# Kernel tuning notes

Hardware: AMD Instinct MI355X
Metric: run time of the kernel (lower is better)

Reference implementation:

```python
import jax, jax.numpy as jnp
import numpy as np

B, S, D, H, L, V = 4, 512, 1024, 16, 4, 32000
DH = D // H
LATENT_START, N_LATENT, LATENT_ID = 64, 6, 5


def _ln(x, g, b):
    m = x.mean(-1, keepdims=True)
    v = ((x - m) ** 2).mean(-1, keepdims=True)
    return (x - m) * jax.lax.rsqrt(v + 1e-5) * g + b


def _model(x_emb, pos_ids, pos_emb, Wqkv, Wo, W1, W2, ln1_g, ln1_b, ln2_g, ln2_b, lnf_g, lnf_b, lm_head):
    # x_emb: [B,T,D]; returns (last_hidden [B,T,D] after final LN, logits [B,T,V])
    b, T, _ = x_emb.shape
    x = x_emb + pos_emb[pos_ids]
    causal = jnp.tril(jnp.ones((T, T), bool))
    for l in range(L):
        h = _ln(x, ln1_g[l], ln1_b[l])
        q, k, v = jnp.split(h @ Wqkv[l], 3, axis=-1)
        q = q.reshape(b, T, H, DH).transpose(0, 2, 1, 3)
        k = k.reshape(b, T, H, DH).transpose(0, 2, 1, 3)
        v = v.reshape(b, T, H, DH).transpose(0, 2, 1, 3)
        scores = jnp.einsum('bhqd,bhkd->bhqk', q, k) / np.float32(np.sqrt(DH))
        scores = jnp.where(causal, scores, jnp.float32(-1e9))
        attn = jax.nn.softmax(scores, axis=-1)
        o = jnp.einsum('bhqk,bhkd->bhqd', attn, v).transpose(0, 2, 1, 3).reshape(b, T, D)
        x = x + o @ Wo[l]
        h2 = _ln(x, ln2_g[l], ln2_b[l])
        x = x + jax.nn.gelu(h2 @ W1[l]) @ W2[l]
    hid = _ln(x, lnf_g, lnf_b)  # GPT2 hidden_states[-1] is post ln_f
    return hid, hid @ lm_head


def setup_inputs() -> dict:
    key = jax.random.key(0)
    ks = jax.random.split(key, 10)
    input_ids = jax.random.randint(ks[0], (B, S), 0, V, dtype=jnp.int32)
    input_ids = input_ids.at[:, LATENT_START:LATENT_START + N_LATENT].set(LATENT_ID)
    attention_mask = jnp.ones((B, S), jnp.int32)
    labels = jax.random.randint(ks[1], (B, S), 0, V, dtype=jnp.int32)
    position_ids = jnp.broadcast_to(jnp.arange(S, dtype=jnp.int32), (B, S))
    s = 0.02
    return {
        'input_ids': input_ids, 'attention_mask': attention_mask,
        'labels': labels, 'position_ids': position_ids,
        'emb': jax.random.normal(ks[2], (V, D), jnp.float32) * s,
        'pos_emb': jax.random.normal(ks[3], (S, D), jnp.float32) * s,
        'Wqkv': jax.random.normal(ks[4], (L, D, 3 * D), jnp.float32) * s,
        'Wo': jax.random.normal(ks[5], (L, D, D), jnp.float32) * s,
        'W1': jax.random.normal(ks[6], (L, D, 4 * D), jnp.float32) * s,
        'W2': jax.random.normal(ks[7], (L, 4 * D, D), jnp.float32) * s,
        'ln1_g': jnp.ones((L, D), jnp.float32), 'ln1_b': jnp.zeros((L, D), jnp.float32),
        'ln2_g': jnp.ones((L, D), jnp.float32), 'ln2_b': jnp.zeros((L, D), jnp.float32),
        'lnf_g': jnp.ones((D,), jnp.float32), 'lnf_b': jnp.zeros((D,), jnp.float32),
        'lm_head': jax.random.normal(ks[8], (D, V), jnp.float32) * s,
    }


def reference(input_ids, attention_mask, labels, position_ids, emb, pos_emb, Wqkv, Wo, W1, W2, ln1_g, ln1_b, ln2_g, ln2_b, lnf_g, lnf_b, lm_head):
    params = (pos_emb, Wqkv, Wo, W1, W2, ln1_g, ln1_b, ln2_g, ln2_b, lnf_g, lnf_b, lm_head)
    inputs_embeds = emb[input_ids]  # [B,S,D]
    start, end = 0, LATENT_START
    logits_list = []
    for p in range(N_LATENT):  # iterative latent passes
        hid, lg = _model(inputs_embeds[:, :end], position_ids[:, :end], *params)
        logits_list.append(lg[:, start:end])
        pos = LATENT_START + p
        # vectorized scatter: splice previous-position hidden state into latent slot
        inputs_embeds = inputs_embeds.at[:, pos, :].set(hid[:, pos - 1, :])
        start, end = end, (S if p + 1 >= N_LATENT else end + 1)
    hid, lg = _model(inputs_embeds[:, :end], position_ids[:, :end], *params)
    logits_list.append(lg[:, start:end])
    logits = jnp.concatenate(logits_list, axis=1)  # [B,S,V]
    shift_logits = logits[:, :-1]
    shift_labels = labels[:, 1:]
    logp = jax.nn.log_softmax(shift_logits, axis=-1)
    loss = -jnp.take_along_axis(logp, shift_labels[..., None], axis=-1).mean()
    return loss, inputs_embeds, logits
```

## Files before the change

kernel.cpp:

```cpp
#include <hip/hip_runtime.h>

static constexpr int BB  = 4;
static constexpr int SS  = 512;
static constexpr int DD  = 1024;
static constexpr int HH  = 16;
static constexpr int LL  = 4;
static constexpr int VV  = 32000;
static constexpr int DHH = 64;
static constexpr int FFF = 4096;

typedef short bf16x8  __attribute__((ext_vector_type(8)));
typedef short bf16x4v __attribute__((ext_vector_type(4)));
typedef float f32x4   __attribute__((ext_vector_type(4)));

__device__ __forceinline__ float b2f(ushort u){
  union { float f; unsigned int u32; } x; x.u32 = ((unsigned int)u) << 16; return x.f;
}
__device__ __forceinline__ ushort f2b(float f){
  union { float f; unsigned int u32; } x; x.f = f;
  unsigned int u = x.u32;
  return (ushort)((u + 0x7FFFu + ((u >> 16) & 1u)) >> 16);
}

__global__ __launch_bounds__(256) void convT_k(const float* __restrict__ in, ushort* __restrict__ out,
                                               int K, int N, long inStride, long outStride)
{
  in  += (long)blockIdx.z * inStride;
  out += (long)blockIdx.z * outStride;
  __shared__ float tile[64][65];
  int n0 = blockIdx.x * 64, k0 = blockIdx.y * 64;
  int tid = threadIdx.x;
  int cc = tid & 63, rr = tid >> 6;
#pragma unroll
  for (int i = 0; i < 16; i++){
    int r = rr + i * 4;
    tile[r][cc] = in[(long)(k0 + r) * N + n0 + cc];
  }
  __syncthreads();
#pragma unroll
  for (int i = 0; i < 16; i++){
    int r = rr + i * 4;
    out[(long)(n0 + r) * K + k0 + cc] = f2b(tile[cc][r]);
  }
}

__global__ __launch_bounds__(256) void embed_k(const int* __restrict__ ids, const float* __restrict__ emb,
                                               const float* __restrict__ pe, float* __restrict__ x,
                                               float* __restrict__ oemb)
{
  int t = blockIdx.x, b = blockIdx.y, tid = threadIdx.x;
  int id = ids[b * SS + t];
  float4 ev = *((const float4*)(emb + (long)id * DD) + tid);
  float4 pv = *((const float4*)(pe  + (long)t  * DD) + tid);
  *((float4*)(x + (long)(t * BB + b) * DD) + tid) =
      make_float4(ev.x + pv.x, ev.y + pv.y, ev.z + pv.z, ev.w + pv.w);
  float* op = oemb + ((long)b * SS + t) * DD + tid * 4;
  op[0] = ev.x; op[1] = ev.y; op[2] = ev.z; op[3] = ev.w;
}

__global__ __launch_bounds__(256) void ln_k(const float* __restrict__ xin, const float* __restrict__ g,
                                            const float* __restrict__ bt, ushort* __restrict__ out, long row0)
{
  long row = row0 + blockIdx.x;
  int tid = threadIdx.x;
  const float* rp = xin + row * DD;
  float4 v = *(const float4*)(rp + tid * 4);
  float s1 = v.x + v.y + v.z + v.w;
  float s2 = v.x * v.x + v.y * v.y + v.z * v.z + v.w * v.w;
#pragma unroll
  for (int o = 32; o; o >>= 1){ s1 += __shfl_down(s1, o); s2 += __shfl_down(s2, o); }
  __shared__ float red[2][4];
  int wv = tid >> 6, lane = tid & 63;
  if (lane == 0){ red[0][wv] = s1; red[1][wv] = s2; }
  __syncthreads();
  s1 = red[0][0] + red[0][1] + red[0][2] + red[0][3];
  s2 = red[1][0] + red[1][1] + red[1][2] + red[1][3];
  float mean = s1 * (1.0f / DD);
  float var  = s2 * (1.0f / DD) - mean * mean;
  float rstd = rsqrtf(var + 1e-5f);
  float4 gv = *(const float4*)(g + tid * 4);
  float4 bv = *(const float4*)(bt + tid * 4);
  ushort4 o4;
  o4.x = f2b((v.x - mean) * rstd * gv.x + bv.x);
  o4.y = f2b((v.y - mean) * rstd * gv.y + bv.y);
  o4.z = f2b((v.z - mean) * rstd * gv.z + bv.z);
  o4.w = f2b((v.w - mean) * rstd * gv.w + bv.w);
  *(ushort4*)(out + row * DD + tid * 4) = o4;
}

template<int EPI>
__device__ __forceinline__ void epi_store(float v, int grow, int ocol, void* Cv, int ldc,
                                          const float* Add, int t0, int l,
                                          ushort* kc, ushort* vc, ushort* qb)
{
  if constexpr (EPI == 1){
    float* Cf = (float*)Cv; long idx = (long)grow * ldc + ocol;
    Cf[idx] = v + Add[idx];
  } else if constexpr (EPI == 2){
    ushort* Cb = (ushort*)Cv; long idx = (long)grow * ldc + ocol;
    float tt = 0.7978845608028654f * (v + 0.044715f * v * v * v);
    Cb[idx] = f2b(0.5f * v * (1.0f + tanhf(tt)));
  } else if constexpr (EPI == 3){
    int t = t0 + (grow >> 2), b = grow & 3;
    ((float*)Cv)[((long)b * SS + t) * VV + ocol] = v;
  } else if constexpr (EPI == 4){
    if (ocol < DD){
      qb[((long)(t0 * BB + grow)) * DD + ocol] = f2b(v);
    } else {
      int t = t0 + (grow >> 2), b = grow & 3;
      int h = (ocol >> 6) & 15, d = ocol & 63;
      long dst = (((long)l * BB + b) * HH + h) * ((long)SS * DHH) + (long)t * DHH + d;
      if (ocol >= 2 * DD) vc[dst] = f2b(v); else kc[dst] = f2b(v);
    }
  }
}

template<int EPI>
__global__ __launch_bounds__(256) void gemm_k(const ushort* __restrict__ A, int lda,
                                              const ushort* __restrict__ BT,
                                              void* Cv, int ldc,
                                              const float* Add,
                                              int M, int N, int K, int gx,
                                              int l, int t0,
                                              ushort* kc, ushort* vc, ushort* qb,
                                              float* part, int KS)
{
  constexpr int BM  = 128;
  constexpr int MFR = 4;
  constexpr int NFR = 4;
  __shared__ ushort As[BM][72];
  __shared__ ushort Bs[128][72];
  int tid = threadIdx.x;
  int wv = tid >> 6, lane = tid & 63;
  int wm = wv >> 1, wn = wv & 1;

  int nwg = gridDim.x, orig = blockIdx.x;
  int wgid;
  if (nwg <= 1024){
    int qq = nwg >> 3, rr8 = nwg & 7, xcd = orig & 7;
    wgid = ((xcd < rr8) ? xcd * (qq + 1) : rr8 * (qq + 1) + (xcd - rr8) * qq) + (orig >> 3);
  } else {
    wgid = orig;
  }

  int gxy = gx * (N >> 7);
  int ksId = wgid / gxy;
  int rem  = wgid - ksId * gxy;
  int bx = rem % gx, by = rem / gx;
  int m0 = bx * BM, n0 = by * 128;
  int Kc = K / KS;
  int k_beg = ksId * Kc, k_end = k_beg + Kc;

  f32x4 acc[MFR][NFR];
  f32x4 zz = {0.f, 0.f, 0.f, 0.f};
#pragma unroll
  for (int m = 0; m < MFR; m++)
#pragma unroll
    for (int n = 0; n < NFR; n++) acc[m][n] = zz;

  int g4 = (lane >> 4) * 4;
  int rA = lane & 15;
  int arow = tid >> 3;
  int acol = (tid & 7) * 8;

  const ushort* Bp = BT + (long)(n0 + arow) * K + acol;
  long sB = 32 * (long)K;
  int gr0 = m0 + arow;       if (gr0 > M - 1) gr0 = M - 1;
  int gr1 = m0 + 32 + arow;  if (gr1 > M - 1) gr1 = M - 1;
  int gr2 = m0 + 64 + arow;  if (gr2 > M - 1) gr2 = M - 1;
  int gr3 = m0 + 96 + arow;  if (gr3 > M - 1) gr3 = M - 1;
  const ushort* Ap0 = A + (long)gr0 * lda + acol;
  const ushort* Ap1 = A + (long)gr1 * lda + acol;
  const ushort* Ap2 = A + (long)gr2 * lda + acol;
  const ushort* Ap3 = A + (long)gr3 * lda + acol;

  uint4 b0 = *(const uint4*)(Bp + k_beg);
  uint4 b1 = *(const uint4*)(Bp + sB + k_beg);
  uint4 b2 = *(const uint4*)(Bp + 2 * sB + k_beg);
  uint4 b3 = *(const uint4*)(Bp + 3 * sB + k_beg);
  uint4 a0 = *(const uint4*)(Ap0 + k_beg);
  uint4 a1 = *(const uint4*)(Ap1 + k_beg);
  uint4 a2 = *(const uint4*)(Ap2 + k_beg);
  uint4 a3 = *(const uint4*)(Ap3 + k_beg);

  for (int k0 = k_beg; k0 < k_end; k0 += 64){
    *(uint4*)&Bs[arow     ][acol] = b0;
    *(uint4*)&Bs[arow + 32][acol] = b1;
    *(uint4*)&Bs[arow + 64][acol] = b2;
    *(uint4*)&Bs[arow + 96][acol] = b3;
    *(uint4*)&As[arow     ][acol] = a0;
    *(uint4*)&As[arow + 32][acol] = a1;
    *(uint4*)&As[arow + 64][acol] = a2;
    *(uint4*)&As[arow + 96][acol] = a3;
    __syncthreads();
    int kn = k0 + 64;
    if (kn < k_end){
      b0 = *(const uint4*)(Bp + kn);
      b1 = *(const uint4*)(Bp + sB + kn);
      b2 = *(const uint4*)(Bp + 2 * sB + kn);
      b3 = *(const uint4*)(Bp + 3 * sB + kn);
      a0 = *(const uint4*)(Ap0 + kn);
      a1 = *(const uint4*)(Ap1 + kn);
      a2 = *(const uint4*)(Ap2 + kn);
      a3 = *(const uint4*)(Ap3 + kn);
    }
#pragma unroll
    for (int kk = 0; kk < 64; kk += 32){
      bf16x8 af[MFR], bfr[NFR];
#pragma unroll
      for (int m = 0; m < MFR; m++){
        int row = wm * 64 + m * 16 + rA;
        bf16x4v lo = *(const bf16x4v*)&As[row][kk + g4];
        bf16x4v hi = *(const bf16x4v*)&As[row][kk + 16 + g4];
        af[m] = __builtin_shufflevector(lo, hi, 0, 1, 2, 3, 4, 5, 6, 7);
      }
#pragma unroll
      for (int n = 0; n < NFR; n++){
        int row = wn * 64 + n * 16 + rA;
        bf16x4v lo = *(const bf16x4v*)&Bs[row][kk + g4];
        bf16x4v hi = *(const bf16x4v*)&Bs[row][kk + 16 + g4];
        bfr[n] = __builtin_shufflevector(lo, hi, 0, 1, 2, 3, 4, 5, 6, 7);
      }
#pragma unroll
      for (int m = 0; m < MFR; m++)
#pragma unroll
        for (int n = 0; n < NFR; n++)
          acc[m][n] = __builtin_amdgcn_mfma_f32_16x16x32_bf16(af[m], bfr[n], acc[m][n], 0, 0, 0);
    }
    __syncthreads();
  }

  int r4 = (lane >> 4) * 4;
#pragma unroll
  for (int m = 0; m < MFR; m++){
#pragma unroll
    for (int n = 0; n < NFR; n++){
      int orow = wm * 64 + m * 16 + r4;
      int ocol = n0 + wn * 64 + n * 16 + rA;
#pragma unroll
      for (int r = 0; r < 4; r++){
        int grow = m0 + orow + r;
        if (grow < M){
          if (KS > 1)
            part[(long)ksId * M * N + (long)grow * N + ocol] = acc[m][n][r];
          else
            epi_store<EPI>(acc[m][n][r], grow, ocol, Cv, ldc, Add, t0, l, kc, vc, qb);
        }
      }
    }
  }
}

template<int EPI>
__global__ __launch_bounds__(256) void sred_k(const float* __restrict__ part, int KS, int M, int N,
                                              void* Cv, int ldc, const float* Add,
                                              int l, int t0, ushort* kc, ushort* vc, ushort* qb)
{
  long i = (long)blockIdx.x * 256 + threadIdx.x;
  long MN = (long)M * N;
  if (i >= MN) return;
  float v = 0.f;
  for (int s = 0; s < KS; s++) v += part[s * MN + i];
  int m = (int)(i / N), n = (int)(i - (long)m * N);
  epi_store<EPI>(v, m, n, Cv, ldc, Add, t0, l, kc, vc, qb);
}

template<int TYPE>
__global__ __launch_bounds__(256) void dec_gemv_k(const float* xf, const ushort* ab,
                                                  const float* g, const float* bt,
                                                  const ushort* WT, float* x,
                                                  ushort* qb, ushort* kc, ushort* vc, ushort* gb,
                                                  int l, int pos)
{
  constexpr int K   = (TYPE == 3) ? FFF : DD;
  constexpr int NCH = K / 1024;
  int tid = threadIdx.x, wid = tid >> 6, lane = tid & 63;
  int n = blockIdx.x * 4 + wid;

  float acc[4] = {0.f, 0.f, 0.f, 0.f};

#pragma unroll
  for (int ch = 0; ch < NCH; ch++){
    int ks = ch * 1024 + lane * 16;
    float a[4][16];
    if constexpr (TYPE == 0 || TYPE == 2){
#pragma unroll
      for (int r = 0; r < 4; r++){
        const float* rp = xf + (long)(pos * BB + r) * DD + ks;
#pragma unroll
        for (int q = 0; q < 4; q++){
          float4 v = *(const float4*)(rp + q * 4);
          a[r][q*4+0] = v.x; a[r][q*4+1] = v.y; a[r][q*4+2] = v.z; a[r][q*4+3] = v.w;
        }
      }
      float gj[16], bj[16];
#pragma unroll
      for (int q = 0; q < 4; q++){
        float4 gv = *(const float4*)(g  + ks + q * 4);
        float4 bv = *(const float4*)(bt + ks + q * 4);
        gj[q*4+0]=gv.x; gj[q*4+1]=gv.y; gj[q*4+2]=gv.z; gj[q*4+3]=gv.w;
        bj[q*4+0]=bv.x; bj[q*4+1]=bv.y; bj[q*4+2]=bv.z; bj[q*4+3]=bv.w;
      }
#pragma unroll
      for (int r = 0; r < 4; r++){
        float s1 = 0.f, s2 = 0.f;
#pragma unroll
        for (int j = 0; j < 16; j++){ s1 += a[r][j]; s2 += a[r][j] * a[r][j]; }
#pragma unroll
        for (int o = 32; o; o >>= 1){ s1 += __shfl_xor(s1, o); s2 += __shfl_xor(s2, o); }
        float mean = s1 * (1.0f / DD);
        float var  = s2 * (1.0f / DD) - mean * mean;
        float rstd = rsqrtf(var + 1e-5f);
#pragma unroll
        for (int j = 0; j < 16; j++)
          a[r][j] = b2f(f2b((a[r][j] - mean) * rstd * gj[j] + bj[j]));
      }
    } else {
      constexpr int AD = (TYPE == 3) ? FFF : DD;
#pragma unroll
      for (int r = 0; r < 4; r++){
        const ushort* rp = ab + (long)(pos * BB + r) * AD + ks;
        uint4 pa = *(const uint4*)rp;
        uint4 pb = *(const uint4*)(rp + 8);
        const unsigned int w[8] = {pa.x, pa.y, pa.z, pa.w, pb.x, pb.y, pb.z, pb.w};
#pragma unroll
        for (int q = 0; q < 8; q++){
          a[r][q*2]   = b2f((ushort)(w[q] & 0xffff));
          a[r][q*2+1] = b2f((ushort)(w[q] >> 16));
        }
      }
    }
    {
      const ushort* wp = WT + (long)n * K + ks;
      uint4 pa = *(const uint4*)wp;
      uint4 pb = *(const uint4*)(wp + 8);
      const unsigned int w[8] = {pa.x, pa.y, pa.z, pa.w, pb.x, pb.y, pb.z, pb.w};
      float wf[16];
#pragma unroll
      for (int q = 0; q < 8; q++){
        wf[q*2]   = b2f((ushort)(w[q] & 0xffff));
        wf[q*2+1] = b2f((ushort)(w[q] >> 16));
      }
#pragma unroll
      for (int r = 0; r < 4; r++){
        float s = 0.f;
#pragma unroll
        for (int j = 0; j < 16; j++) s += a[r][j] * wf[j];
        acc[r] += s;
      }
    }
  }

#pragma unroll
  for (int r = 0; r < 4; r++)
#pragma unroll
    for (int o = 32; o; o >>= 1) acc[r] += __shfl_xor(acc[r], o);

  if (lane < 4){
    int r = lane;
    long Rrow = (long)(pos * BB + r);
    float v = acc[r];
    if constexpr (TYPE == 0){
      if (n < DD){
        qb[Rrow * DD + n] = f2b(v);
      } else if (n < 2 * DD){
        int h = (n - DD) >> 6, d = n & 63;
        kc[(((long)l * BB + r) * HH + h) * ((long)SS * DHH) + (long)pos * DHH + d] = f2b(v);
      } else {
        int h = (n - 2 * DD) >> 6, d = n & 63;
        vc[(((long)l * BB + r) * HH + h) * ((long)SS * DHH) + (long)pos * DHH + d] = f2b(v);
      }
    } else if constexpr (TYPE == 2){
      float tt = 0.7978845608028654f * (v + 0.044715f * v * v * v);
      gb[Rrow * FFF + n] = f2b(0.5f * v * (1.0f + tanhf(tt)));
    } else {
      long idx = Rrow * DD + n;
      x[idx] = x[idx] + v;
    }
  }
}

__global__ __launch_bounds__(256) void dec_final_k(const float* xf, const float* g, const float* bt,
                                                   const float* pe, ushort* hid, float* x,
                                                   float* oemb, int pos)
{
  int wid = threadIdx.x >> 6, lane = threadIdx.x & 63;
  long R = (long)(pos * BB + wid);
  const float* rp = xf + R * DD + lane * 16;
  float a[16];
#pragma unroll
  for (int q = 0; q < 4; q++){
    float4 v = *(const float4*)(rp + q * 4);
    a[q*4+0] = v.x; a[q*4+1] = v.y; a[q*4+2] = v.z; a[q*4+3] = v.w;
  }
  float s1 = 0.f, s2 = 0.f;
#pragma unroll
  for (int j = 0; j < 16; j++){ s1 += a[j]; s2 += a[j] * a[j]; }
#pragma unroll
  for (int o = 32; o; o >>= 1){ s1 += __shfl_xor(s1, o); s2 += __shfl_xor(s2, o); }
  float mean = s1 * (1.0f / DD);
  float var  = s2 * (1.0f / DD) - mean * mean;
  float rstd = rsqrtf(var + 1e-5f);
  int pn = pos + 1;
#pragma unroll
  for (int j = 0; j < 16; j++){
    int d = lane * 16 + j;
    ushort hb = f2b((a[j] - mean) * rstd * g[d] + bt[d]);
    hid[R * DD + d] = hb;
    float hv = b2f(hb);
    oemb[((long)wid * SS + pn) * DD + d] = hv;
    x[((long)(pn * BB + wid)) * DD + d] = hv + pe[(long)pn * DD + d];
  }
}

__global__ __launch_bounds__(256) void attn_k(const ushort* __restrict__ qb, const ushort* __restrict__ kc,
                                              const ushort* __restrict__ vc, ushort* __restrict__ o,
                                              int l, int t0, int Tc)
{
  __shared__ float sc[4][512];
  __shared__ float qs[4][64];
  int tid = threadIdx.x, wv = tid >> 6, lane = tid & 63;
  int b = blockIdx.z, h = blockIdx.y;
  int qrow = blockIdx.x * 4 + wv;
  bool act = qrow < Tc;
  int tq = t0 + qrow;
  long kvoff = (((long)l * BB + b) * HH + h) * ((long)SS * DHH);
  const ushort* kb = kc + kvoff;
  const ushort* vb = vc + kvoff;
  if (act) qs[wv][lane] = b2f(qb[((long)(tq * BB + b)) * DD + h * DHH + lane]);
  __syncthreads();
  int nk = act ? (tq + 1) : 0;
  float m = -3.0e38f;
  for (int key = lane; key < nk; key += 64){
    const ushort* kp = kb + (long)key * DHH;
    float s = 0.f;
#pragma unroll
    for (int j = 0; j < 8; j++){
      uint4 kvv = *(const uint4*)(kp + j * 8);
      s += qs[wv][j*8+0] * b2f((ushort)(kvv.x & 0xffff));
      s += qs[wv][j*8+1] * b2f((ushort)(kvv.x >> 16));
      s += qs[wv][j*8+2] * b2f((ushort)(kvv.y & 0xffff));
      s += qs[wv][j*8+3] * b2f((ushort)(kvv.y >> 16));
      s += qs[wv][j*8+4] * b2f((ushort)(kvv.z & 0xffff));
      s += qs[wv][j*8+5] * b2f((ushort)(kvv.z >> 16));
      s += qs[wv][j*8+6] * b2f((ushort)(kvv.w & 0xffff));
      s += qs[wv][j*8+7] * b2f((ushort)(kvv.w >> 16));
    }
    s *= 0.125f;
    sc[wv][key] = s;
    m = fmaxf(m, s);
  }
#pragma unroll
  for (int off = 32; off; off >>= 1) m = fmaxf(m, __shfl_xor(m, off));
  float ssum = 0.f;
  for (int key = lane; key < nk; key += 64){
    float p = expf(sc[wv][key] - m);
    sc[wv][key] = p;
    ssum += p;
  }
#pragma unroll
  for (int off = 32; off; off >>= 1) ssum += __shfl_xor(ssum, off);
  __syncthreads();
  float accv = 0.f;
  int key = 0;
  for (; key + 3 < nk; key += 4){
    float p0 = sc[wv][key],     p1 = sc[wv][key + 1];
    float p2 = sc[wv][key + 2], p3 = sc[wv][key + 3];
    float v0 = b2f(vb[(long)key * DHH + lane]);
    float v1 = b2f(vb[(long)(key + 1) * DHH + lane]);
    float v2 = b2f(vb[(long)(key + 2) * DHH + lane]);
    float v3 = b2f(vb[(long)(key + 3) * DHH + lane]);
    accv += p0 * v0 + p1 * v1 + p2 * v2 + p3 * v3;
  }
  for (; key < nk; key++)
    accv += sc[wv][key] * b2f(vb[(long)key * DHH + lane]);
  if (act) o[((long)(tq * BB + b)) * DD + h * DHH + lane] = f2b(accv / ssum);
}

__global__ __launch_bounds__(256) void advance_k(const ushort* __restrict__ hid, const float* __restrict__ pe,
                                                 float* __restrict__ x, float* __restrict__ oemb, int pos)
{
  int d = blockIdx.x * 256 + threadIdx.x;
  int b = blockIdx.y;
  float hv = b2f(hid[((long)((pos - 1) * BB + b)) * DD + d]);
  oemb[((long)b * SS + pos) * DD + d] = hv;
  x[((long)(pos * BB + b)) * DD + d] = hv + pe[(long)pos * DD + d];
}

__global__ __launch_bounds__(256) void loss_rows_k(const float* __restrict__ logits, const int* __restrict__ labels,
                                                   float* __restrict__ rowloss)
{
  int t = blockIdx.x, b = blockIdx.y, tid = threadIdx.x;
  const float* row = logits + ((long)b * SS + t) * VV;
  float m = -3.0e38f, s = 0.f;
  for (int i = tid; i < VV; i += 256){
    float v = row[i];
    if (v > m){ s = s * expf(m - v) + 1.f; m = v; }
    else s += expf(v - m);
  }
#pragma unroll
  for (int off = 32; off; off >>= 1){
    float om = __shfl_xor(m, off), os = __shfl_xor(s, off);
    float nm = fmaxf(m, om);
    s = s * expf(m - nm) + os * expf(om - nm);
    m = nm;
  }
  __shared__ float sm[4], ssb[4];
  if ((tid & 63) == 0){ sm[tid >> 6] = m; ssb[tid >> 6] = s; }
  __syncthreads();
  if (tid == 0){
    float M = fmaxf(fmaxf(sm[0], sm[1]), fmaxf(sm[2], sm[3]));
    float S = ssb[0] * expf(sm[0] - M) + ssb[1] * expf(sm[1] - M)
            + ssb[2] * expf(sm[2] - M) + ssb[3] * expf(sm[3] - M);
    int lab = labels[b * SS + t + 1];
    rowloss[b * (SS - 1) + t] = (M + logf(S)) - row[lab];
  }
}

__global__ __launch_bounds__(256) void loss_final_k(const float* __restrict__ rowloss, float* __restrict__ out)
{
  int tid = threadIdx.x;
  float s = 0.f;
  for (int i = tid; i < BB * (SS - 1); i += 256) s += rowloss[i];
#pragma unroll
  for (int o = 32; o; o >>= 1) s += __shfl_down(s, o);
  __shared__ float red[4];
  if ((tid & 63) == 0) red[tid >> 6] = s;
  __syncthreads();
  if (tid == 0) out[0] = (red[0] + red[1] + red[2] + red[3]) / (float)(BB * (SS - 1));
}

static inline int cdiv_i(int a, int b){ return (a + b - 1) / b; }

extern "C" void kernel_launch(void* const* d_in, const int* in_sizes, int n_in,
                              void* d_out, int out_size, void* d_ws, size_t ws_size,
                              hipStream_t stream)
{
  (void)in_sizes; (void)n_in; (void)out_size; (void)ws_size;
  const int*   ids    = (const int*)d_in[0];
  const int*   labels = (const int*)d_in[2];
  const float* emb    = (const float*)d_in[4];
  const float* pe     = (const float*)d_in[5];
  const float* Wqkv   = (const float*)d_in[6];
  const float* Wo     = (const float*)d_in[7];
  const float* W1     = (const float*)d_in[8];
  const float* W2     = (const float*)d_in[9];
  const float* ln1g   = (const float*)d_in[10];
  const float* ln1b   = (const float*)d_in[11];
  const float* ln2g   = (const float*)d_in[12];
  const float* ln2b   = (const float*)d_in[13];
  const float* lnfg   = (const float*)d_in[14];
  const float* lnfb   = (const float*)d_in[15];
  const float* lm     = (const float*)d_in[16];

  float* out_loss   = (float*)d_out;
  float* out_emb    = out_loss + 1;
  float* out_logits = out_emb + (size_t)BB * SS * DD;

  char* wsp = (char*)d_ws;
  size_t off = 0;
  auto alloc = [&](size_t bytes) -> void* {
    void* p = wsp + off; off += (bytes + 255) & ~(size_t)255; return p;
  };
  ushort* wqkvT = (ushort*)alloc((size_t)LL * 3 * DD * DD * 2);
  ushort* woT   = (ushort*)alloc((size_t)LL * DD * DD * 2);
  ushort* w1T   = (ushort*)alloc((size_t)LL * FFF * DD * 2);
  ushort* w2T   = (ushort*)alloc((size_t)LL * DD * FFF * 2);
  ushort* lmT   = (ushort*)alloc((size_t)VV * DD * 2);
  float*  x     = (float*)alloc((size_t)BB * SS * DD * 4);
  ushort* hbuf  = (ushort*)alloc((size_t)BB * SS * DD * 2);
  ushort* qbuf  = (ushort*)alloc((size_t)BB * SS * DD * 2);
  ushort* obuf  = (ushort*)alloc((size_t)BB * SS * DD * 2);
  ushort* gbuf  = (ushort*)alloc((size_t)BB * SS * FFF * 2);
  ushort* hid   = (ushort*)alloc((size_t)BB * SS * DD * 2);
  ushort* kcache= (ushort*)alloc((size_t)LL * BB * SS * DD * 2);
  ushort* vcache= (ushort*)alloc((size_t)LL * BB * SS * DD * 2);
  float*  part  = (float*)alloc((size_t)17 * 1024 * 1024);
  float*  rowls = (float*)alloc((size_t)BB * (SS - 1) * 4);

  convT_k<<<dim3(3 * DD / 64, DD / 64, LL), dim3(256), 0, stream>>>(Wqkv, wqkvT, DD, 3 * DD, (long)DD * 3 * DD, (long)3 * DD * DD);
  convT_k<<<dim3(DD / 64, DD / 64, LL),     dim3(256), 0, stream>>>(Wo,   woT,  DD, DD,     (long)DD * DD,     (long)DD * DD);
  convT_k<<<dim3(FFF / 64, DD / 64, LL),    dim3(256), 0, stream>>>(W1,   w1T,  DD, FFF,    (long)DD * FFF,    (long)FFF * DD);
  convT_k<<<dim3(DD / 64, FFF / 64, LL),    dim3(256), 0, stream>>>(W2,   w2T,  FFF, DD,    (long)FFF * DD,    (long)DD * FFF);
  convT_k<<<dim3(VV / 64, DD / 64, 1),      dim3(256), 0, stream>>>(lm,   lmT,  DD, VV,     0, 0);

  embed_k<<<dim3(SS, BB), dim3(256), 0, stream>>>(ids, emb, pe, x, out_emb);

  const int ct0[7] = {0, 64, 65, 66, 67, 68, 69};
  const int ct1[7] = {64, 65, 66, 67, 68, 69, 512};

  auto g128 = [&](int epi, const ushort* A, int lda, const ushort* BT, void* C, int ldc,
                  const float* Add, int M, int N, int K, int l, int t0, int KS){
    int gx = cdiv_i(M, 128);
    int nwg = gx * (N >> 7) * KS;
    if (epi == 1) gemm_k<1><<<nwg, 256, 0, stream>>>(A, lda, BT, C, ldc, Add, M, N, K, gx, l, t0, kcache, vcache, qbuf, part, KS);
    if (epi == 2) gemm_k<2><<<nwg, 256, 0, stream>>>(A, lda, BT, C, ldc, Add, M, N, K, gx, l, t0, kcache, vcache, qbuf, part, KS);
    if (epi == 3) gemm_k<3><<<nwg, 256, 0, stream>>>(A, lda, BT, C, ldc, Add, M, N, K, gx, l, t0, kcache, vcache, qbuf, part, KS);
    if (epi == 4) gemm_k<4><<<nwg, 256, 0, stream>>>(A, lda, BT, C, ldc, Add, M, N, K, gx, l, t0, kcache, vcache, qbuf, part, KS);
    if (KS > 1){
      int nred = cdiv_i(M * N, 256);
      if (epi == 1) sred_k<1><<<nred, 256, 0, stream>>>(part, KS, M, N, C, ldc, Add, l, t0, kcache, vcache, qbuf);
      if (epi == 2) sred_k<2><<<nred, 256, 0, stream>>>(part, KS, M, N, C, ldc, Add, l, t0, kcache, vcache, qbuf);
      if (epi == 4) sred_k<4><<<nred, 256, 0, stream>>>(part, KS, M, N, C, ldc, Add, l, t0, kcache, vcache, qbuf);
    }
  };

  for (int c = 0; c < 7; c++){
    int t0 = ct0[c];
    int Tc = ct1[c] - t0;
    int M  = Tc * BB;
    long roff = (long)t0 * BB;

    if (Tc == 1){
      int pos = t0;
      for (int l = 0; l < LL; l++){
        dec_gemv_k<0><<<dim3(3 * DD / 4), dim3(256), 0, stream>>>(x, nullptr, ln1g + l * DD, ln1b + l * DD,
            wqkvT + (long)l * 3 * DD * DD, nullptr, qbuf, kcache, vcache, nullptr, l, pos);
        attn_k<<<dim3(1, HH, BB), dim3(64), 0, stream>>>(qbuf, kcache, vcache, obuf, l, t0, Tc);
        dec_gemv_k<1><<<dim3(DD / 4), dim3(256), 0, stream>>>(nullptr, obuf, nullptr, nullptr,
            woT + (long)l * DD * DD, x, nullptr, nullptr, nullptr, nullptr, l, pos);
        dec_gemv_k<2><<<dim3(FFF / 4), dim3(256), 0, stream>>>(x, nullptr, ln2g + l * DD, ln2b + l * DD,
            w1T + (long)l * FFF * DD, nullptr, nullptr, nullptr, nullptr, gbuf, l, pos);
        dec_gemv_k<3><<<dim3(DD / 4), dim3(256), 0, stream>>>(nullptr, gbuf, nullptr, nullptr,
            w2T + (long)l * DD * FFF, x, nullptr, nullptr, nullptr, nullptr, l, pos);
      }
      dec_final_k<<<dim3(1), dim3(256), 0, stream>>>(x, lnfg, lnfb, pe, hid, x, out_emb, pos);
    } else {
      bool small = (M <= 256);
      int ksQKV = small ? 4 : 1;
      int ksWO  = small ? 8 : 2;
      int ksW1  = small ? 4 : 1;
      int ksW2  = small ? 8 : 2;
      for (int l = 0; l < LL; l++){
        ln_k<<<dim3(M), dim3(256), 0, stream>>>(x, ln1g + l * DD, ln1b + l * DD, hbuf, roff);
        g128(4, hbuf + roff * DD, DD, wqkvT + (long)l * 3 * DD * DD, nullptr, 0, nullptr, M, 3 * DD, DD, l, t0, ksQKV);
        attn_k<<<dim3(cdiv_i(Tc, 4), HH, BB), dim3(256), 0, stream>>>(qbuf, kcache, vcache, obuf, l, t0, Tc);
        g128(1, obuf + roff * DD, DD, woT + (long)l * DD * DD, x + roff * DD, DD, x + roff * DD, M, DD, DD, l, t0, ksWO);
        ln_k<<<dim3(M), dim3(256), 0, stream>>>(x, ln2g + l * DD, ln2b + l * DD, hbuf, roff);
        g128(2, hbuf + roff * DD, DD, w1T + (long)l * FFF * DD, gbuf + roff * FFF, FFF, nullptr, M, FFF, DD, l, t0, ksW1);
        g128(1, gbuf + roff * FFF, FFF, w2T + (long)l * DD * FFF, x + roff * DD, DD, x + roff * DD, M, DD, FFF, l, t0, ksW2);
      }
      ln_k<<<dim3(M), dim3(256), 0, stream>>>(x, lnfg, lnfb, hid, roff);
      if (c == 0)
        advance_k<<<dim3(DD / 256, BB), dim3(256), 0, stream>>>(hid, pe, x, out_emb, 64);
    }
  }

  g128(3, hid, DD, lmT, out_logits, 0, nullptr, BB * SS, VV, DD, 0, 0, 1);

  loss_rows_k<<<dim3(SS - 1, BB), dim3(256), 0, stream>>>(out_logits, labels, rowls);
  loss_final_k<<<dim3(1), dim3(256), 0, stream>>>(rowls, out_loss);
}
```

Before: 2.852 ms.

## Process four query rows per wave in attention to reuse K/V loads

The attention kernel now gives each wavefront four consecutive query rows, so a block covers 16 queries and the grid along queries shrinks by four. Each K vector and V element loaded from global memory is reused across four dot products and four accumulators, which cuts redundant K/V traffic. Causal masking inside the shared key range is done by writing -1e9 scores for keys past each row's limit. The cost is four times the shared memory per block, which may lower occupancy, plus extra register pressure.

```diff
diff --git a/kernel.cpp b/kernel.cpp
--- a/kernel.cpp
+++ b/kernel.cpp
@@ -417,64 +417,100 @@
                                               const ushort* __restrict__ vc, ushort* __restrict__ o,
                                               int l, int t0, int Tc)
 {
-  __shared__ float sc[4][512];
-  __shared__ float qs[4][64];
+  __shared__ float sc[4][4][512];
+  __shared__ float qs[4][4][64];
   int tid = threadIdx.x, wv = tid >> 6, lane = tid & 63;
   int b = blockIdx.z, h = blockIdx.y;
-  int qrow = blockIdx.x * 4 + wv;
-  bool act = qrow < Tc;
-  int tq = t0 + qrow;
+  int q0 = blockIdx.x * 16 + wv * 4;
   long kvoff = (((long)l * BB + b) * HH + h) * ((long)SS * DHH);
   const ushort* kb = kc + kvoff;
   const ushort* vb = vc + kvoff;
-  if (act) qs[wv][lane] = b2f(qb[((long)(tq * BB + b)) * DD + h * DHH + lane]);
+
+#pragma unroll
+  for (int r = 0; r < 4; r++){
+    int qrow = q0 + r;
+    float qv = 0.f;
+    if (qrow < Tc) qv = b2f(qb[((long)((t0 + qrow) * BB + b)) * DD + h * DHH + lane]);
+    qs[wv][r][lane] = qv;
+  }
   __syncthreads();
-  int nk = act ? (tq + 1) : 0;
-  float m = -3.0e38f;
-  for (int key = lane; key < nk; key += 64){
+
+  int nk_r[4];
+#pragma unroll
+  for (int r = 0; r < 4; r++) nk_r[r] = (q0 + r < Tc) ? (t0 + q0 + r + 1) : 0;
+  int qlast = (q0 + 3 < Tc) ? q0 + 3 : Tc - 1;
+  int nkmax = (q0 < Tc) ? (t0 + qlast + 1) : 0;
+
+  float m[4] = {-3.0e38f, -3.0e38f, -3.0e38f, -3.0e38f};
+  for (int key = lane; key < nkmax; key += 64){
     const ushort* kp = kb + (long)key * DHH;
-    float s = 0.f;
+    float s0 = 0.f, s1 = 0.f, s2 = 0.f, s3 = 0.f;
 #pragma unroll
     for (int j = 0; j < 8; j++){
       uint4 kvv = *(const uint4*)(kp + j * 8);
-      s += qs[wv][j*8+0] * b2f((ushort)(kvv.x & 0xffff));
-      s += qs[wv][j*8+1] * b2f((ushort)(kvv.x >> 16));
-      s += qs[wv][j*8+2] * b2f((ushort)(kvv.y & 0xffff));
-      s += qs[wv][j*8+3] * b2f((ushort)(kvv.y >> 16));
-      s += qs[wv][j*8+4] * b2f((ushort)(kvv.z & 0xffff));
-      s += qs[wv][j*8+5] * b2f((ushort)(kvv.z >> 16));
-      s += qs[wv][j*8+6] * b2f((ushort)(kvv.w & 0xffff));
-      s += qs[wv][j*8+7] * b2f((ushort)(kvv.w >> 16));
-    }
-    s *= 0.125f;
-    sc[wv][key] = s;
-    m = fmaxf(m, s);
-  }
-#pragma unroll
-  for (int off = 32; off; off >>= 1) m = fmaxf(m, __shfl_xor(m, off));
-  float ssum = 0.f;
-  for (int key = lane; key < nk; key += 64){
-    float p = expf(sc[wv][key] - m);
-    sc[wv][key] = p;
-    ssum += p;
-  }
-#pragma unroll
-  for (int off = 32; off; off >>= 1) ssum += __shfl_xor(ssum, off);
+      const unsigned int w[4] = {kvv.x, kvv.y, kvv.z, kvv.w};
+#pragma unroll
+      for (int q = 0; q < 4; q++){
+        float k0f = b2f((ushort)(w[q] & 0xffff));
+        float k1f = b2f((ushort)(w[q] >> 16));
+        int e = j * 8 + q * 2;
+        s0 += qs[wv][0][e] * k0f + qs[wv][0][e+1] * k1f;
+        s1 += qs[wv][1][e] * k0f + qs[wv][1][e+1] * k1f;
+        s2 += qs[wv][2][e] * k0f + qs[wv][2][e+1] * k1f;
+        s3 += qs[wv][3][e] * k0f + qs[wv][3][e+1] * k1f;
+      }
+    }
+    float sv[4] = {s0 * 0.125f, s1 * 0.125f, s2 * 0.125f, s3 * 0.125f};
+#pragma unroll
+    for (int r = 0; r < 4; r++){
+      float vmask = (key < nk_r[r]) ? sv[r] : -1.0e9f;
+      sc[wv][r][key] = vmask;
+      m[r] = fmaxf(m[r], vmask);
+    }
+  }
+#pragma unroll
+  for (int r = 0; r < 4; r++)
+#pragma unroll
+    for (int off = 32; off; off >>= 1) m[r] = fmaxf(m[r], __shfl_xor(m[r], off));
+
+  float ssum[4] = {0.f, 0.f, 0.f, 0.f};
+  for (int key = lane; key < nkmax; key += 64){
+#pragma unroll
+    for (int r = 0; r < 4; r++){
+      float p = expf(sc[wv][r][key] - m[r]);
+      sc[wv][r][key] = p;
+      ssum[r] += p;
+    }
+  }
+#pragma unroll
+  for (int r = 0; r < 4; r++)
+#pragma unroll
+    for (int off = 32; off; off >>= 1) ssum[r] += __shfl_xor(ssum[r], off);
   __syncthreads();
-  float accv = 0.f;
+
+  float accv[4] = {0.f, 0.f, 0.f, 0.f};
   int key = 0;
-  for (; key + 3 < nk; key += 4){
-    float p0 = sc[wv][key],     p1 = sc[wv][key + 1];
-    float p2 = sc[wv][key + 2], p3 = sc[wv][key + 3];
+  for (; key + 3 < nkmax; key += 4){
     float v0 = b2f(vb[(long)key * DHH + lane]);
     float v1 = b2f(vb[(long)(key + 1) * DHH + lane]);
     float v2 = b2f(vb[(long)(key + 2) * DHH + lane]);
     float v3 = b2f(vb[(long)(key + 3) * DHH + lane]);
-    accv += p0 * v0 + p1 * v1 + p2 * v2 + p3 * v3;
-  }
-  for (; key < nk; key++)
-    accv += sc[wv][key] * b2f(vb[(long)key * DHH + lane]);
-  if (act) o[((long)(tq * BB + b)) * DD + h * DHH + lane] = f2b(accv / ssum);
+#pragma unroll
+    for (int r = 0; r < 4; r++)
+      accv[r] += sc[wv][r][key] * v0 + sc[wv][r][key+1] * v1
+               + sc[wv][r][key+2] * v2 + sc[wv][r][key+3] * v3;
+  }
+  for (; key < nkmax; key++){
+    float v0 = b2f(vb[(long)key * DHH + lane]);
+#pragma unroll
+    for (int r = 0; r < 4; r++) accv[r] += sc[wv][r][key] * v0;
+  }
+#pragma unroll
+  for (int r = 0; r < 4; r++){
+    int qrow = q0 + r;
+    if (qrow < Tc)
+      o[((long)((t0 + qrow) * BB + b)) * DD + h * DHH + lane] = f2b(accv[r] / ssum[r]);
+  }
 }
 
 __global__ __launch_bounds__(256) void advance_k(const ushort* __restrict__ hid, const float* __restrict__ pe,
@@ -634,7 +670,7 @@
       for (int l = 0; l < LL; l++){
         ln_k<<<dim3(M), dim3(256), 0, stream>>>(x, ln1g + l * DD, ln1b + l * DD, hbuf, roff);
         g128(4, hbuf + roff * DD, DD, wqkvT + (long)l * 3 * DD * DD, nullptr, 0, nullptr, M, 3 * DD, DD, l, t0, ksQKV);
-        attn_k<<<dim3(cdiv_i(Tc, 4), HH, BB), dim3(256), 0, stream>>>(qbuf, kcache, vcache, obuf, l, t0, Tc);
+        attn_k<<<dim3(cdiv_i(Tc, 16), HH, BB), dim3(256), 0, stream>>>(qbuf, kcache, vcache, obuf, l, t0, Tc);
         g128(1, obuf + roff * DD, DD, woT + (long)l * DD * DD, x + roff * DD, DD, x + roff * DD, M, DD, DD, l, t0, ksWO);
         ln_k<<<dim3(M), dim3(256), 0, stream>>>(x, ln2g + l * DD, ln2b + l * DD, hbuf, roff);
         g128(2, hbuf + roff * DD, DD, w1T + (long)l * FFF * DD, gbuf + roff * FFF, FFF, nullptr, M, FFF, DD, l, t0, ksW1);
```

After: 2.897 ms. No clear change (+1.6%).
